# Performance work log

Hardware: AMD Instinct MI355X
Metric: run time of the kernel (lower is better)

The kernel has to match this reference:

```python
import jax, jax.numpy as jnp
import numpy as np

B, N, H, D = 4, 2048, 8, 64
DM = 512  # model dim = H * D


def setup_inputs() -> dict:
    key = jax.random.key(0)
    ks = jax.random.split(key, 8)
    x = jax.random.normal(ks[0], (B, N, DM), dtype=jnp.float32)
    mask_k = jax.random.randint(ks[1], (B, N), 0, 5) > 0
    mask_q = jax.random.randint(ks[2], (B, N), 0, 5) > 0
    s_in = 1.0 / np.sqrt(DM)
    s_out = 1.0 / np.sqrt(H * D)
    Wq = jax.random.normal(ks[3], (DM, H * D), dtype=jnp.float32) * s_in
    Wk = jax.random.normal(ks[4], (DM, H * D), dtype=jnp.float32) * s_in
    Wv = jax.random.normal(ks[5], (DM, H * D), dtype=jnp.float32) * s_in
    Wo = jax.random.normal(ks[6], (H * D, DM), dtype=jnp.float32) * s_out
    bo = jnp.zeros((DM,), dtype=jnp.float32)
    return {"x": x, "Wq": Wq, "Wk": Wk, "Wv": Wv, "Wo": Wo, "bo": bo,
            "mask_k": mask_k, "mask_q": mask_q}


def reference(x, Wq, Wk, Wv, Wo, bo, mask_k, mask_q):
    b, n, _ = x.shape
    # projections (no bias), split into heads: b n (h d) -> b n h d
    q = (x @ Wq).reshape(b, n, H, D)
    k = (x @ Wk).reshape(b, n, H, D)
    v = (x @ Wv).reshape(b, n, H, D)
    scale = D ** (-0.5)
    sim = jnp.einsum('bihd,bjhd->bijh', q, k) * scale  # [b, i, j, h]
    big_neg = jnp.finfo(jnp.float32).min
    sim = jnp.where(mask_k[:, None, :, None], sim, big_neg)
    sim = jnp.where(mask_q[:, :, None, None], sim, big_neg)
    attn = jax.nn.softmax(sim, axis=-2)  # softmax over key axis j
    out = jnp.einsum('bijh,bjhd->bihd', attn, v).reshape(b, n, H * D)
    return out @ Wo + bo
```

## Files before the change

kernel.cpp:

```cpp
#include <hip/hip_runtime.h>

typedef _Float16 f16;
typedef __fp16   fp16x2 __attribute__((ext_vector_type(2)));
typedef _Float16 f16x8 __attribute__((ext_vector_type(8)));
typedef float    f32x4 __attribute__((ext_vector_type(4)));

#define MFMA16(A, B, C) __builtin_amdgcn_mfma_f32_16x16x32_f16((A), (B), (C), 0, 0, 0)

__device__ __forceinline__ void gl_lds16(const void* g, void* l) {
  __builtin_amdgcn_global_load_lds(
      (const __attribute__((address_space(1))) void*)g,
      (__attribute__((address_space(3))) void*)l, 16, 0, 0);
}

static constexpr size_t OFF_XH  = 0;
static constexpr size_t OFF_WQT = 8388608;
static constexpr size_t OFF_WOT = OFF_WQT + 3 * 524288;
static constexpr size_t OFF_QH  = OFF_WOT + 524288;
static constexpr size_t OFF_KH  = OFF_QH + 8388608;
static constexpr size_t OFF_VT  = OFF_KH + 8388608;
static constexpr size_t OFF_A2  = OFF_VT + 8388608;
static constexpr size_t OFF_AMK = OFF_A2 + 8388608;

#define QSCALE 0.18033688011112042f
#define NEGFIX -11.541560327111708f

__global__ void k_cvt_x(const float* __restrict__ x, f16* __restrict__ xh,
                        const int* __restrict__ mask_k, float* __restrict__ amk) {
  int i = blockIdx.x * blockDim.x + threadIdx.x;
  const float4* p = (const float4*)x + (size_t)i * 2;
  float4 a = p[0], b = p[1];
  f16x8 o = { (f16)a.x, (f16)a.y, (f16)a.z, (f16)a.w,
              (f16)b.x, (f16)b.y, (f16)b.z, (f16)b.w };
  *((f16x8*)xh + i) = o;
  if (i < 8192) amk[i] = mask_k[i] ? 0.0f : -1000.0f;
}

__global__ void k_cvt_w4(const float* __restrict__ w0, const float* __restrict__ w1,
                         const float* __restrict__ w2, const float* __restrict__ w3,
                         f16* __restrict__ dst) {
  __shared__ float tile[32][33];
  const int z = blockIdx.z;
  const float* w = (z == 0) ? w0 : (z == 1) ? w1 : (z == 2) ? w2 : w3;
  const float sc = (z == 0) ? QSCALE : 1.0f;
  f16* wt = dst + (size_t)z * 262144;
  int tx = threadIdx.x & 31, ty = threadIdx.x >> 5;
  int bx = blockIdx.x, by = blockIdx.y;
#pragma unroll
  for (int i = 0; i < 32; i += 8)
    tile[ty + i][tx] = w[(size_t)(by * 32 + ty + i) * 512 + bx * 32 + tx];
  __syncthreads();
#pragma unroll
  for (int i = 0; i < 32; i += 8)
    wt[(size_t)(bx * 32 + ty + i) * 512 + by * 32 + tx] = (f16)(tile[tx][ty + i] * sc);
}

template <int MODE, int BM, int BN>
__global__ __launch_bounds__(256, (MODE == 2 ? 3 : 2))
void k_gemm(const f16* __restrict__ A, const f16* __restrict__ Bt,
            void* __restrict__ O0, void* __restrict__ O1, void* __restrict__ O2,
            const float* __restrict__ bias) {
  constexpr int MR = BM / 32, NF = BN / 32;
  constexpr int AP = BM / 32, BP = BN / 32;
  constexpr int ABYTES = BM * 128;
  constexpr int BBYTES = BN * 128;
  constexpr int SM_STAGE  = 2 * (ABYTES + BBYTES);
  constexpr int SM_BOUNCE = (MODE == 3) ? 128 * 136 * 2 : 0;
  constexpr int SM = SM_STAGE > SM_BOUNCE ? SM_STAGE : SM_BOUNCE;
  __shared__ __align__(16) char smem[SM];
  const int t = threadIdx.x;
  const int lane = t & 63, w = t >> 6;
  const int wr = w >> 1, wc = w & 1;
  const int l15 = lane & 15, l4 = lane >> 4;
  const int lr = lane >> 3, lc = lane & 7;
  const int flat = blockIdx.x + gridDim.x * blockIdx.y;
  const int nwg  = gridDim.x * gridDim.y;
  const int sw   = (flat & 7) * (nwg >> 3) + (flat >> 3);
  const int row0 = (sw / gridDim.x) * BM;
  const int col0 = (sw % gridDim.x) * BN;

  f32x4 acc[MR][NF] = {};

  auto stage = [&](int kt, int buf) {
    char* dA = smem + buf * ABYTES + w * 1024;
    char* dB = smem + 2 * ABYTES + buf * BBYTES + w * 1024;
#pragma unroll
    for (int p = 0; p < AP; ++p) {
      int r = p * 32 + w * 8 + lr;
      gl_lds16((const char*)A + ((size_t)(row0 + r) * 512 + kt) * 2 + ((lc ^ (r & 7)) << 4),
               dA + p * 4096);
    }
#pragma unroll
    for (int p = 0; p < BP; ++p) {
      int r = p * 32 + w * 8 + lr;
      gl_lds16((const char*)Bt + ((size_t)(col0 + r) * 512 + kt) * 2 + ((lc ^ (r & 7)) << 4),
               dB + p * 4096);
    }
  };

  stage(0, 0);
  for (int ks = 0; ks < 8; ++ks) {
    const int buf = ks & 1;
    __syncthreads();
    if (ks < 7) stage((ks + 1) * 64, buf ^ 1);
    const char* cA = smem + buf * ABYTES;
    const char* cB = smem + 2 * ABYTES + buf * BBYTES;
    __builtin_amdgcn_s_setprio(1);
#pragma unroll
    for (int kb = 0; kb < 2; ++kb) {
      f16x8 af[MR], bf[NF];
#pragma unroll
      for (int m = 0; m < MR; ++m) {
        int r = wr * (BM / 2) + m * 16 + l15;
        int lb = r * 128 + kb * 64 + l4 * 16;
        af[m] = *(const f16x8*)(cA + (lb ^ ((r & 7) << 4)));
      }
#pragma unroll
      for (int n = 0; n < NF; ++n) {
        int r = wc * (BN / 2) + n * 16 + l15;
        int lb = r * 128 + kb * 64 + l4 * 16;
        bf[n] = *(const f16x8*)(cB + (lb ^ ((r & 7) << 4)));
      }
#pragma unroll
      for (int m = 0; m < MR; ++m)
#pragma unroll
        for (int n = 0; n < NF; ++n)
          acc[m][n] = MFMA16(af[m], bf[n], acc[m][n]);
    }
    __builtin_amdgcn_s_setprio(0);
  }

  if (MODE == 2) {
#pragma unroll
    for (int m = 0; m < MR; ++m)
#pragma unroll
      for (int n = 0; n < NF; ++n) {
        int gr = row0 + wr * (BM / 2) + m * 16 + l4 * 4;
        int gc = col0 + wc * (BN / 2) + n * 16 + l15;
        float* C = (float*)O0;
        float bv = bias[gc];
#pragma unroll
        for (int rr = 0; rr < 4; ++rr)
          C[(size_t)(gr + rr) * 512 + gc] = acc[m][n][rr] + bv;
      }
  } else {
    int seg = col0 >> 9;
    if (seg < 2) {
      __syncthreads();
      f16* bb = (f16*)smem;
#pragma unroll
      for (int m = 0; m < MR; ++m)
#pragma unroll
        for (int n = 0; n < NF; ++n) {
          int r = wr * (BM / 2) + m * 16 + l4 * 4;
          int c = wc * (BN / 2) + n * 16 + l15;
#pragma unroll
          for (int rr = 0; rr < 4; ++rr)
            bb[(r + rr) * 136 + c] = (f16)acc[m][n][rr];
        }
      __syncthreads();
      f16* C = (f16*)(seg == 0 ? O0 : O1);
      int cbase = col0 & 511;
#pragma unroll
      for (int i = 0; i < 8; ++i) {
        int idx = i * 256 + t;
        int r = idx >> 4, c8 = (idx & 15) * 8;
        uint4 v = *(const uint4*)(bb + r * 136 + c8);
        *(uint4*)(C + (size_t)(row0 + r) * 512 + cbase + c8) = v;
      }
    } else {
#pragma unroll
      for (int m = 0; m < MR; ++m)
#pragma unroll
        for (int n = 0; n < NF; ++n) {
          int gr = row0 + wr * (BM / 2) + m * 16 + l4 * 4;
          int lcol = (col0 & 511) + wc * (BN / 2) + n * 16 + l15;
          f16* C = (f16*)O2;
          int hh = lcol >> 6, dd = lcol & 63;
          int bb2 = gr >> 11, ns = gr & 2047;
          union { uint2 u2; f16 v[4]; } pk;
#pragma unroll
          for (int rr = 0; rr < 4; ++rr) pk.v[rr] = (f16)acc[m][n][rr];
          *(uint2*)(C + (size_t)((bb2 * 8 + hh) * 64 + dd) * 2048 + ns) = pk.u2;
        }
    }
  }
}

__global__ __launch_bounds__(256, 2)
void k_attn(const f16* __restrict__ Q, const f16* __restrict__ K,
            const f16* __restrict__ Vt, const float* __restrict__ amk,
            const int* __restrict__ mask_q, f16* __restrict__ A2) {
  __shared__ __align__(16) f16 sK[2][128 * 64];
  __shared__ __align__(16) f16 sV[2][64 * 128];
  __shared__ __align__(16) f16 sP[4][32 * 64];
  const int t = threadIdx.x, lane = t & 63, w = t >> 6;
  const int l15 = lane & 15, l4 = lane >> 4;
  const int lr = lane >> 3, lc = lane & 7;
  const int sw = (blockIdx.x & 7) * 64 + (blockIdx.x >> 3);
  const int qx = sw & 15, bh = sw >> 4;
  const int b = bh >> 3, h = bh & 7;
  const int q0 = qx * 128 + w * 32;

  f16x8 qa[2][2];
  float qm[2], qo[2];
#pragma unroll
  for (int g = 0; g < 2; ++g) {
    const f16* qb = Q + (size_t)(b * 2048 + q0 + g * 16 + l15) * 512 + h * 64 + l4 * 8;
    qa[g][0] = *(const f16x8*)qb;
    qa[g][1] = *(const f16x8*)(qb + 32);
    int mq = mask_q[b * 2048 + q0 + g * 16 + l15];
    qm[g] = mq ? 1.0f : 0.0f;
    qo[g] = mq ? 0.0f : -8.0f;
  }

  const f16x8 onesv = { (f16)1.f, (f16)1.f, (f16)1.f, (f16)1.f,
                        (f16)1.f, (f16)1.f, (f16)1.f, (f16)1.f };
  f32x4 o[2][4] = {};
  f32x4 oex[2] = {};

  const char* Kbase  = (const char*)K + ((size_t)b * 2048 * 512 + h * 64) * 2;
  const char* VtBase = (const char*)Vt + ((size_t)(b * 8 + h) * 64) * 2048 * 2;
  const float* amkb = amk + b * 2048;
  char* sPw = (char*)&sP[w][0];

  auto stage = [&](int kv, int buf) {
#pragma unroll
    for (int p = 0; p < 4; ++p) {
      int r = p * 32 + w * 8 + lr;
      gl_lds16(Kbase + (size_t)(kv + r) * 1024 + ((lc ^ (r & 7)) << 4),
               (char*)&sK[buf][0] + p * 4096 + w * 1024);
    }
#pragma unroll
    for (int p = 0; p < 4; ++p) {
      int d = p * 16 + w * 4 + (lane >> 4);
      int c = lane & 15;
      gl_lds16(VtBase + ((size_t)d * 2048 + kv) * 2 + ((c ^ (d & 7)) << 4),
               (char*)&sV[buf][0] + p * 4096 + w * 1024);
    }
  };

  stage(0, 0);
  for (int it = 0; it < 16; ++it) {
    const int kv = it * 128, buf = it & 1;
    __syncthreads();
    if (it < 15) stage(kv + 128, buf ^ 1);
    const char* cK = (const char*)&sK[buf][0];
    const char* cV = (const char*)&sV[buf][0];

#pragma unroll
    for (int h2 = 0; h2 < 2; ++h2) {
      f32x4 sT[2][4];
      __builtin_amdgcn_s_setprio(1);
#pragma unroll
      for (int jf = 0; jf < 4; ++jf) {
        int r = h2 * 64 + jf * 16 + l15;
        int base = r * 128 + l4 * 16;
        f16x8 k0 = *(const f16x8*)(cK + (base ^ ((r & 7) << 4)));
        f16x8 k1 = *(const f16x8*)(cK + ((base + 64) ^ ((r & 7) << 4)));
#pragma unroll
        for (int g = 0; g < 2; ++g) {
          f32x4 z = { NEGFIX, NEGFIX, NEGFIX, NEGFIX };
          z = MFMA16(k0, qa[g][0], z);
          z = MFMA16(k1, qa[g][1], z);
          sT[g][jf] = z;
        }
      }
      __builtin_amdgcn_s_setprio(0);

      f32x4 amv[4];
#pragma unroll
      for (int jf = 0; jf < 4; ++jf)
        amv[jf] = *(const f32x4*)(amkb + kv + h2 * 64 + jf * 16 + l4 * 4);
#pragma unroll
      for (int g = 0; g < 2; ++g)
#pragma unroll
        for (int jf = 0; jf < 4; ++jf) {
          float p0 = __builtin_amdgcn_exp2f(
              __builtin_fmaf(amv[jf][0], qm[g],
                  __builtin_fmaf(sT[g][jf][0], qm[g], qo[g])));
          float p1 = __builtin_amdgcn_exp2f(
              __builtin_fmaf(amv[jf][1], qm[g],
                  __builtin_fmaf(sT[g][jf][1], qm[g], qo[g])));
          float p2 = __builtin_amdgcn_exp2f(
              __builtin_fmaf(amv[jf][2], qm[g],
                  __builtin_fmaf(sT[g][jf][2], qm[g], qo[g])));
          float p3 = __builtin_amdgcn_exp2f(
              __builtin_fmaf(amv[jf][3], qm[g],
                  __builtin_fmaf(sT[g][jf][3], qm[g], qo[g])));
          fp16x2 a01 = __builtin_amdgcn_cvt_pkrtz(p0, p1);
          fp16x2 a23 = __builtin_amdgcn_cvt_pkrtz(p2, p3);
          uint2 pk = { __builtin_bit_cast(unsigned, a01),
                       __builtin_bit_cast(unsigned, a23) };
          int row = g * 16 + l15;
          int boff = row * 128 + jf * 32 + l4 * 8;
          *(uint2*)(sPw + (boff ^ ((row & 7) << 4))) = pk;
        }

      __builtin_amdgcn_s_setprio(1);
#pragma unroll
      for (int kb = 0; kb < 2; ++kb) {
        f16x8 pa[2];
#pragma unroll
        for (int g = 0; g < 2; ++g) {
          int rq = g * 16 + l15;
          int pbase = rq * 128 + kb * 64 + l4 * 16;
          pa[g] = *(const f16x8*)(sPw + (pbase ^ ((rq & 7) << 4)));
          oex[g] = MFMA16(pa[g], onesv, oex[g]);
        }
#pragma unroll
        for (int df = 0; df < 4; ++df) {
          int d = df * 16 + l15;
          int vbase = d * 256 + h2 * 128 + kb * 64 + l4 * 16;
          f16x8 bv = *(const f16x8*)(cV + (vbase ^ ((d & 7) << 4)));
#pragma unroll
          for (int g = 0; g < 2; ++g)
            o[g][df] = MFMA16(pa[g], bv, o[g][df]);
        }
      }
      __builtin_amdgcn_s_setprio(0);
    }
  }

#pragma unroll
  for (int g = 0; g < 2; ++g) {
    float inv[4];
#pragma unroll
    for (int rr = 0; rr < 4; ++rr) inv[rr] = 1.0f / oex[g][rr];
#pragma unroll
    for (int df = 0; df < 4; ++df)
#pragma unroll
      for (int rr = 0; rr < 4; ++rr)
        A2[(size_t)(b * 2048 + q0 + g * 16 + l4 * 4 + rr) * 512 + h * 64 + df * 16 + l15] =
            (f16)(o[g][df][rr] * inv[rr]);
  }
}

extern "C" void kernel_launch(void* const* d_in, const int* in_sizes, int n_in,
                              void* d_out, int out_size, void* d_ws, size_t ws_size,
                              hipStream_t stream) {
  (void)in_sizes; (void)n_in; (void)out_size; (void)ws_size;
  const float* x   = (const float*)d_in[0];
  const float* Wq  = (const float*)d_in[1];
  const float* Wk  = (const float*)d_in[2];
  const float* Wv  = (const float*)d_in[3];
  const float* Wo  = (const float*)d_in[4];
  const float* bo  = (const float*)d_in[5];
  const int* mask_k = (const int*)d_in[6];
  const int* mask_q = (const int*)d_in[7];
  float* out = (float*)d_out;
  char* ws = (char*)d_ws;

  f16* Xh   = (f16*)(ws + OFF_XH);
  f16* Wqkv = (f16*)(ws + OFF_WQT);
  f16* Wot  = (f16*)(ws + OFF_WOT);
  f16* Qh   = (f16*)(ws + OFF_QH);
  f16* Kh   = (f16*)(ws + OFF_KH);
  f16* Vt   = (f16*)(ws + OFF_VT);
  f16* A2   = (f16*)(ws + OFF_A2);
  float* AMK = (float*)(ws + OFF_AMK);

  k_cvt_x<<<2048, 256, 0, stream>>>(x, Xh, mask_k, AMK);
  k_cvt_w4<<<dim3(16, 16, 4), 256, 0, stream>>>(Wq, Wk, Wv, Wo, Wqkv);

  k_gemm<3, 128, 128><<<dim3(12, 64), 256, 0, stream>>>(Xh, Wqkv, Qh, Kh, Vt, nullptr);

  k_attn<<<512, 256, 0, stream>>>(Qh, Kh, Vt, AMK, mask_q, A2);

  k_gemm<2, 128, 64><<<dim3(8, 64), 256, 0, stream>>>(A2, Wot, out, nullptr, nullptr, bo);
}
```

Baseline: 158.7 us.

## Handle masked queries via precomputed V mean and shrink attention KV tile

Fully masked query rows get a uniform softmax, so their output is just the mean of V over all keys. A new small kernel precomputes that per-(batch, head, dim) mean, and the attention epilogue writes it for masked rows. This removes the per-element query-mask FMAs from the exp path. The KV tile also shrinks from 128 to 64 keys per iteration, which halves LDS use and raises the launch-bounds occupancy target from 2 to 3. The trade-offs are an extra kernel launch, twice as many barrier/stage iterations, and an occupancy gain that may not matter with 512 blocks.

```diff
diff --git a/kernel.cpp b/kernel.cpp
--- a/kernel.cpp
+++ b/kernel.cpp
@@ -21,6 +21,7 @@
 static constexpr size_t OFF_VT  = OFF_KH + 8388608;
 static constexpr size_t OFF_A2  = OFF_VT + 8388608;
 static constexpr size_t OFF_AMK = OFF_A2 + 8388608;
+static constexpr size_t OFF_VM  = OFF_AMK + 32768;
 
 #define QSCALE 0.18033688011112042f
 #define NEGFIX -11.541560327111708f
@@ -53,6 +54,22 @@
 #pragma unroll
   for (int i = 0; i < 32; i += 8)
     wt[(size_t)(bx * 32 + ty + i) * 512 + by * 32 + tx] = (f16)(tile[tx][ty + i] * sc);
+}
+
+__global__ void k_vmean(const f16* __restrict__ Vt, float* __restrict__ vm) {
+  int row = blockIdx.x * 4 + (threadIdx.x >> 6);
+  int lane = threadIdx.x & 63;
+  const f16x8* p = (const f16x8*)(Vt + (size_t)row * 2048) + lane;
+  float s = 0.f;
+#pragma unroll
+  for (int i = 0; i < 4; ++i) {
+    f16x8 v = p[i * 64];
+#pragma unroll
+    for (int e = 0; e < 8; ++e) s += (float)v[e];
+  }
+#pragma unroll
+  for (int i = 32; i; i >>= 1) s += __shfl_xor(s, i, 64);
+  if (lane == 0) vm[row] = s * (1.0f / 2048.0f);
 }
 
 template <int MODE, int BM, int BN>
@@ -187,12 +204,13 @@
   }
 }
 
-__global__ __launch_bounds__(256, 2)
+__global__ __launch_bounds__(256, 3)
 void k_attn(const f16* __restrict__ Q, const f16* __restrict__ K,
             const f16* __restrict__ Vt, const float* __restrict__ amk,
-            const int* __restrict__ mask_q, f16* __restrict__ A2) {
-  __shared__ __align__(16) f16 sK[2][128 * 64];
-  __shared__ __align__(16) f16 sV[2][64 * 128];
+            const int* __restrict__ mask_q, const float* __restrict__ vmean,
+            f16* __restrict__ A2) {
+  __shared__ __align__(16) f16 sK[2][64 * 64];
+  __shared__ __align__(16) f16 sV[2][64 * 64];
   __shared__ __align__(16) f16 sP[4][32 * 64];
   const int t = threadIdx.x, lane = t & 63, w = t >> 6;
   const int l15 = lane & 15, l4 = lane >> 4;
@@ -203,15 +221,11 @@
   const int q0 = qx * 128 + w * 32;
 
   f16x8 qa[2][2];
-  float qm[2], qo[2];
 #pragma unroll
   for (int g = 0; g < 2; ++g) {
     const f16* qb = Q + (size_t)(b * 2048 + q0 + g * 16 + l15) * 512 + h * 64 + l4 * 8;
     qa[g][0] = *(const f16x8*)qb;
     qa[g][1] = *(const f16x8*)(qb + 32);
-    int mq = mask_q[b * 2048 + q0 + g * 16 + l15];
-    qm[g] = mq ? 1.0f : 0.0f;
-    qo[g] = mq ? 0.0f : -8.0f;
   }
 
   const f16x8 onesv = { (f16)1.f, (f16)1.f, (f16)1.f, (f16)1.f,
@@ -226,113 +240,108 @@
 
   auto stage = [&](int kv, int buf) {
 #pragma unroll
-    for (int p = 0; p < 4; ++p) {
+    for (int p = 0; p < 2; ++p) {
       int r = p * 32 + w * 8 + lr;
       gl_lds16(Kbase + (size_t)(kv + r) * 1024 + ((lc ^ (r & 7)) << 4),
                (char*)&sK[buf][0] + p * 4096 + w * 1024);
     }
 #pragma unroll
-    for (int p = 0; p < 4; ++p) {
-      int d = p * 16 + w * 4 + (lane >> 4);
-      int c = lane & 15;
-      gl_lds16(VtBase + ((size_t)d * 2048 + kv) * 2 + ((c ^ (d & 7)) << 4),
+    for (int p = 0; p < 2; ++p) {
+      int d = p * 32 + w * 8 + lr;
+      gl_lds16(VtBase + ((size_t)d * 2048 + kv) * 2 + ((lc ^ (d & 7)) << 4),
                (char*)&sV[buf][0] + p * 4096 + w * 1024);
     }
   };
 
   stage(0, 0);
-  for (int it = 0; it < 16; ++it) {
-    const int kv = it * 128, buf = it & 1;
+  for (int it = 0; it < 32; ++it) {
+    const int kv = it * 64, buf = it & 1;
     __syncthreads();
-    if (it < 15) stage(kv + 128, buf ^ 1);
+    if (it < 31) stage(kv + 64, buf ^ 1);
     const char* cK = (const char*)&sK[buf][0];
     const char* cV = (const char*)&sV[buf][0];
 
-#pragma unroll
-    for (int h2 = 0; h2 < 2; ++h2) {
-      f32x4 sT[2][4];
-      __builtin_amdgcn_s_setprio(1);
+    f32x4 amv[4];
+#pragma unroll
+    for (int jf = 0; jf < 4; ++jf)
+      amv[jf] = *(const f32x4*)(amkb + kv + jf * 16 + l4 * 4);
+
+    f32x4 sT[2][4];
+    __builtin_amdgcn_s_setprio(1);
+#pragma unroll
+    for (int jf = 0; jf < 4; ++jf) {
+      int r = jf * 16 + l15;
+      int base = r * 128 + l4 * 16;
+      f16x8 k0 = *(const f16x8*)(cK + (base ^ ((r & 7) << 4)));
+      f16x8 k1 = *(const f16x8*)(cK + ((base + 64) ^ ((r & 7) << 4)));
+#pragma unroll
+      for (int g = 0; g < 2; ++g) {
+        f32x4 z = { NEGFIX, NEGFIX, NEGFIX, NEGFIX };
+        z = MFMA16(k0, qa[g][0], z);
+        z = MFMA16(k1, qa[g][1], z);
+        sT[g][jf] = z;
+      }
+    }
+    __builtin_amdgcn_s_setprio(0);
+
+#pragma unroll
+    for (int g = 0; g < 2; ++g)
 #pragma unroll
       for (int jf = 0; jf < 4; ++jf) {
-        int r = h2 * 64 + jf * 16 + l15;
-        int base = r * 128 + l4 * 16;
-        f16x8 k0 = *(const f16x8*)(cK + (base ^ ((r & 7) << 4)));
-        f16x8 k1 = *(const f16x8*)(cK + ((base + 64) ^ ((r & 7) << 4)));
-#pragma unroll
-        for (int g = 0; g < 2; ++g) {
-          f32x4 z = { NEGFIX, NEGFIX, NEGFIX, NEGFIX };
-          z = MFMA16(k0, qa[g][0], z);
-          z = MFMA16(k1, qa[g][1], z);
-          sT[g][jf] = z;
-        }
-      }
-      __builtin_amdgcn_s_setprio(0);
-
-      f32x4 amv[4];
-#pragma unroll
-      for (int jf = 0; jf < 4; ++jf)
-        amv[jf] = *(const f32x4*)(amkb + kv + h2 * 64 + jf * 16 + l4 * 4);
-#pragma unroll
-      for (int g = 0; g < 2; ++g)
-#pragma unroll
-        for (int jf = 0; jf < 4; ++jf) {
-          float p0 = __builtin_amdgcn_exp2f(
-              __builtin_fmaf(amv[jf][0], qm[g],
-                  __builtin_fmaf(sT[g][jf][0], qm[g], qo[g])));
-          float p1 = __builtin_amdgcn_exp2f(
-              __builtin_fmaf(amv[jf][1], qm[g],
-                  __builtin_fmaf(sT[g][jf][1], qm[g], qo[g])));
-          float p2 = __builtin_amdgcn_exp2f(
-              __builtin_fmaf(amv[jf][2], qm[g],
-                  __builtin_fmaf(sT[g][jf][2], qm[g], qo[g])));
-          float p3 = __builtin_amdgcn_exp2f(
-              __builtin_fmaf(amv[jf][3], qm[g],
-                  __builtin_fmaf(sT[g][jf][3], qm[g], qo[g])));
-          fp16x2 a01 = __builtin_amdgcn_cvt_pkrtz(p0, p1);
-          fp16x2 a23 = __builtin_amdgcn_cvt_pkrtz(p2, p3);
-          uint2 pk = { __builtin_bit_cast(unsigned, a01),
-                       __builtin_bit_cast(unsigned, a23) };
-          int row = g * 16 + l15;
-          int boff = row * 128 + jf * 32 + l4 * 8;
-          *(uint2*)(sPw + (boff ^ ((row & 7) << 4))) = pk;
-        }
-
-      __builtin_amdgcn_s_setprio(1);
-#pragma unroll
-      for (int kb = 0; kb < 2; ++kb) {
-        f16x8 pa[2];
-#pragma unroll
-        for (int g = 0; g < 2; ++g) {
-          int rq = g * 16 + l15;
-          int pbase = rq * 128 + kb * 64 + l4 * 16;
-          pa[g] = *(const f16x8*)(sPw + (pbase ^ ((rq & 7) << 4)));
-          oex[g] = MFMA16(pa[g], onesv, oex[g]);
-        }
-#pragma unroll
-        for (int df = 0; df < 4; ++df) {
-          int d = df * 16 + l15;
-          int vbase = d * 256 + h2 * 128 + kb * 64 + l4 * 16;
-          f16x8 bv = *(const f16x8*)(cV + (vbase ^ ((d & 7) << 4)));
-#pragma unroll
-          for (int g = 0; g < 2; ++g)
-            o[g][df] = MFMA16(pa[g], bv, o[g][df]);
-        }
-      }
-      __builtin_amdgcn_s_setprio(0);
-    }
+        float p0 = __builtin_amdgcn_exp2f(sT[g][jf][0] + amv[jf][0]);
+        float p1 = __builtin_amdgcn_exp2f(sT[g][jf][1] + amv[jf][1]);
+        float p2 = __builtin_amdgcn_exp2f(sT[g][jf][2] + amv[jf][2]);
+        float p3 = __builtin_amdgcn_exp2f(sT[g][jf][3] + amv[jf][3]);
+        fp16x2 a01 = __builtin_amdgcn_cvt_pkrtz(p0, p1);
+        fp16x2 a23 = __builtin_amdgcn_cvt_pkrtz(p2, p3);
+        uint2 pk = { __builtin_bit_cast(unsigned, a01),
+                     __builtin_bit_cast(unsigned, a23) };
+        int row = g * 16 + l15;
+        int boff = row * 128 + jf * 32 + l4 * 8;
+        *(uint2*)(sPw + (boff ^ ((row & 7) << 4))) = pk;
+      }
+
+    __builtin_amdgcn_s_setprio(1);
+#pragma unroll
+    for (int kb = 0; kb < 2; ++kb) {
+      f16x8 pa[2];
+#pragma unroll
+      for (int g = 0; g < 2; ++g) {
+        int rq = g * 16 + l15;
+        int pbase = rq * 128 + kb * 64 + l4 * 16;
+        pa[g] = *(const f16x8*)(sPw + (pbase ^ ((rq & 7) << 4)));
+        oex[g] = MFMA16(pa[g], onesv, oex[g]);
+      }
+#pragma unroll
+      for (int df = 0; df < 4; ++df) {
+        int d = df * 16 + l15;
+        int vbase = d * 128 + kb * 64 + l4 * 16;
+        f16x8 bv = *(const f16x8*)(cV + (vbase ^ ((d & 7) << 4)));
+#pragma unroll
+        for (int g = 0; g < 2; ++g)
+          o[g][df] = MFMA16(pa[g], bv, o[g][df]);
+      }
+    }
+    __builtin_amdgcn_s_setprio(0);
   }
 
 #pragma unroll
   for (int g = 0; g < 2; ++g) {
+    const int4 mq4 = *(const int4*)(mask_q + b * 2048 + q0 + g * 16 + l4 * 4);
+    const int mq[4] = { mq4.x, mq4.y, mq4.z, mq4.w };
     float inv[4];
 #pragma unroll
     for (int rr = 0; rr < 4; ++rr) inv[rr] = 1.0f / oex[g][rr];
 #pragma unroll
-    for (int df = 0; df < 4; ++df)
-#pragma unroll
-      for (int rr = 0; rr < 4; ++rr)
+    for (int df = 0; df < 4; ++df) {
+      float vm = vmean[(b * 8 + h) * 64 + df * 16 + l15];
+#pragma unroll
+      for (int rr = 0; rr < 4; ++rr) {
+        float val = mq[rr] ? (o[g][df][rr] * inv[rr]) : vm;
         A2[(size_t)(b * 2048 + q0 + g * 16 + l4 * 4 + rr) * 512 + h * 64 + df * 16 + l15] =
-            (f16)(o[g][df][rr] * inv[rr]);
+            (f16)val;
+      }
+    }
   }
 }
 
@@ -359,13 +368,16 @@
   f16* Vt   = (f16*)(ws + OFF_VT);
   f16* A2   = (f16*)(ws + OFF_A2);
   float* AMK = (float*)(ws + OFF_AMK);
+  float* VM  = (float*)(ws + OFF_VM);
 
   k_cvt_x<<<2048, 256, 0, stream>>>(x, Xh, mask_k, AMK);
   k_cvt_w4<<<dim3(16, 16, 4), 256, 0, stream>>>(Wq, Wk, Wv, Wo, Wqkv);
 
   k_gemm<3, 128, 128><<<dim3(12, 64), 256, 0, stream>>>(Xh, Wqkv, Qh, Kh, Vt, nullptr);
 
-  k_attn<<<512, 256, 0, stream>>>(Qh, Kh, Vt, AMK, mask_q, A2);
+  k_vmean<<<512, 256, 0, stream>>>(Vt, VM);
+
+  k_attn<<<512, 256, 0, stream>>>(Qh, Kh, Vt, AMK, mask_q, VM, A2);
 
   k_gemm<2, 128, 64><<<dim3(8, 64), 256, 0, stream>>>(A2, Wot, out, nullptr, nullptr, bo);
 }
```

After: 169.3 us. +6.7%, slower.
